# Kernel optimization log

Measured on AMD Instinct MI355X. Metric: run time of the kernel, lower is better.

The kernel has to match this reference:

```python
import jax, jax.numpy as jnp
import numpy as np

N_NODES = 50000
N_EDGES = 800000
EMBED_DIM = 128
VOCAB = 30000
BATCH = 1024
CTX_LEN = 50
NUM_LAYERS = 2
BN_EPS = 1e-5


def setup_inputs() -> dict:
    key = jax.random.key(0)
    ks = jax.random.split(key, 20)
    D = EMBED_DIM
    edge_index = jax.random.randint(ks[0], (2, N_EDGES), 0, N_NODES)
    norm = jax.random.uniform(ks[1], (N_EDGES,), dtype=jnp.float32) * 0.2  # GCN deg^-1/2 * deg^-1/2 weights
    ctx_ids = jax.random.randint(ks[2], (BATCH, CTX_LEN), 0, VOCAB)
    miss_ids = jax.random.randint(ks[3], (BATCH,), 0, VOCAB)
    vocab_to_fg = jnp.where(
        jax.random.uniform(ks[4], (VOCAB,)) < 0.5,
        jax.random.randint(ks[5], (VOCAB,), 0, N_NODES),
        -1,
    )
    emb_table = jax.random.normal(ks[6], (VOCAB, D), dtype=jnp.float32) * 0.02
    emb_table = emb_table.at[0].set(0.0)  # padding_idx=0
    fg_emb = jax.random.normal(ks[7], (N_NODES, D), dtype=jnp.float32) * 0.02
    gc_w = jax.random.normal(ks[8], (NUM_LAYERS, D, D), dtype=jnp.float32) * 0.02
    bn_gamma = jnp.ones((NUM_LAYERS, D), dtype=jnp.float32)
    bn_beta = jnp.zeros((NUM_LAYERS, D), dtype=jnp.float32)
    attn_w = jax.random.normal(ks[9], (D,), dtype=jnp.float32) * 0.02
    attn_b = jnp.zeros((), dtype=jnp.float32)
    fusion_w = jax.random.normal(ks[10], (D, 2 * D), dtype=jnp.float32) * 0.02
    fusion_b = jnp.zeros((D,), dtype=jnp.float32)
    proj1_w = jax.random.normal(ks[11], (2 * D, 2 * D), dtype=jnp.float32) * 0.02
    proj1_b = jnp.zeros((2 * D,), dtype=jnp.float32)
    proj2_w = jax.random.normal(ks[12], (D, 2 * D), dtype=jnp.float32) * 0.02
    proj2_b = jnp.zeros((D,), dtype=jnp.float32)
    return dict(edge_index=edge_index, norm=norm, ctx_ids=ctx_ids, miss_ids=miss_ids,
                vocab_to_fg=vocab_to_fg, emb_table=emb_table, fg_emb=fg_emb, gc_w=gc_w,
                bn_gamma=bn_gamma, bn_beta=bn_beta, attn_w=attn_w, attn_b=attn_b,
                fusion_w=fusion_w, fusion_b=fusion_b, proj1_w=proj1_w, proj1_b=proj1_b,
                proj2_w=proj2_w, proj2_b=proj2_b)


def reference(edge_index, norm, ctx_ids, miss_ids, vocab_to_fg, emb_table, fg_emb,
              gc_w, bn_gamma, bn_beta, attn_w, attn_b, fusion_w, fusion_b,
              proj1_w, proj1_b, proj2_w, proj2_b):
    N, D = fg_emb.shape
    row, col = edge_index[0], edge_index[1]
    # --- GCN stack: h <- h + BN(ReLU(Linear(A @ h))) ---
    h = fg_emb
    for l in range(gc_w.shape[0]):
        # sparse adj matmul: out[i] = sum_{(i,j) in E} norm_e * h[j]
        agg = jax.ops.segment_sum(norm[:, None] * h[col], row, num_segments=N)  # [N, D]
        z = jax.nn.relu(agg @ gc_w[l].T)
        mu = jnp.mean(z, axis=0)
        var = jnp.var(z, axis=0)  # biased, matches BN train-mode normalization
        h2 = (z - mu) * jax.lax.rsqrt(var + BN_EPS) * bn_gamma[l] + bn_beta[l]
        h = h + h2  # dropout is identity in eval reference
    graph_embs = h
    # --- context attention pooling ---
    ctx = emb_table[ctx_ids]                      # [B, L, D]
    logits = jnp.einsum('bld,d->bl', ctx, attn_w) + attn_b
    w = jax.nn.softmax(logits, axis=1)
    ctx_emb = jnp.einsum('bl,bld->bd', w, ctx)    # [B, D]
    # --- missing-ingredient embedding: vocab emb fused with gathered graph emb ---
    base = emb_table[miss_ids]                    # [B, D]
    fg_ids = vocab_to_fg[miss_ids]
    mask = fg_ids >= 0
    gp = jnp.where(mask[:, None], graph_embs[jnp.clip(fg_ids, 0)], 0.0)
    miss_emb = jnp.concatenate([base, gp], axis=-1) @ fusion_w.T + fusion_b
    # --- projection MLP ---
    q = jnp.concatenate([ctx_emb, miss_emb], axis=-1)
    q = jax.nn.relu(q @ proj1_w.T + proj1_b)
    query = q @ proj2_w.T + proj2_b
    return query, graph_embs
```

## Files before the change

### kernel.cpp

```cpp
#include <hip/hip_runtime.h>

#define NN 50000
#define NE 800000
#define DIM 128
#define NB 1024
#define CTXL 50
#define BN_EPS 1e-5f
#define STRIPS 3125
#define GEMM_BLOCKS 512
#define NBK 49
#define BCAP 20000
#define ABLK 1024
#define NAB 782

static const size_t OFF_Z    = 0;
static const size_t OFF_AH   = 6400000;
static const size_t OFF_HBF  = 9600000;
static const size_t OFF_EDG  = 12800000;
static const size_t OFF_RS   = 14400000;
static const size_t OFF_SCSH = 14550400;
static const size_t OFF_WH   = 14550656;
static const size_t OFF_WL   = 14567040;
static const size_t OFF_BKT  = OFF_Z + 3200000;
static const size_t OFF_P2   = OFF_Z + 3200000;
static const size_t OFF_ACNT = OFF_AH;
static const size_t OFF_AOFS = OFF_AH + 40000;
static const size_t OFF_BTOT = OFF_AH + 80000;
static const size_t OFF_QIN  = OFF_Z;
static const size_t OFF_CAT  = OFF_Z + 131072;
static const size_t OFF_Q1   = OFF_Z + 262144;
static const size_t OFF_FWB  = OFF_Z + 393216;
static const size_t OFF_P1B  = OFF_Z + 409600;
static const size_t OFF_P2B  = OFF_Z + 442368;

typedef __attribute__((ext_vector_type(8))) short s16x8;
typedef __attribute__((ext_vector_type(4))) float fx4;

__device__ __forceinline__ unsigned short f2bf(float f) {
    unsigned u = __float_as_uint(f);
    unsigned r = u + 0x7FFFu + ((u >> 16) & 1u);
    return (unsigned short)(r >> 16);
}
__device__ __forceinline__ float bf2f(unsigned short b) {
    return __uint_as_float((unsigned)b << 16);
}

__global__ __launch_bounds__(256) void csr_prep_kernel(const int* __restrict__ row,
                                                       const float* __restrict__ W,
                                                       const float* __restrict__ fg,
                                                       int* __restrict__ cnt,
                                                       unsigned short* __restrict__ Wh,
                                                       unsigned short* __restrict__ Wl,
                                                       unsigned short* __restrict__ hbf) {
    int i = blockIdx.x * 256 + threadIdx.x;
    if (i < 2 * DIM * DIM) {
        float v = W[i];
        unsigned short h = f2bf(v);
        Wh[i] = h;
        Wl[i] = f2bf(v - bf2f(h));
    }
    if (i < NN * DIM / 4) {
        float4 v = reinterpret_cast<const float4*>(fg)[i];
        reinterpret_cast<ushort4*>(hbf)[i] =
            make_ushort4(f2bf(v.x), f2bf(v.y), f2bf(v.z), f2bf(v.w));
    }
    if (blockIdx.x < NAB) {
        __shared__ int c[NBK];
        int t = threadIdx.x;
        if (t < NBK) c[t] = 0;
        __syncthreads();
        int base = blockIdx.x * ABLK;
        #pragma unroll
        for (int k = 0; k < 4; k++) {
            int e = base + k * 256 + t;
            if (e < NE) atomicAdd(&c[row[e] >> 10], 1);
        }
        __syncthreads();
        if (t < NBK) cnt[t * 784 + blockIdx.x] = c[t];
    }
}

__global__ __launch_bounds__(1024) void binA_scan(const int* __restrict__ cnt,
                                                  int* __restrict__ ofs,
                                                  int* __restrict__ btot) {
    __shared__ int lds[1024];
    int b = blockIdx.x, t = threadIdx.x;
    int v = (t < NAB) ? cnt[b * 784 + t] : 0;
    lds[t] = v;
    __syncthreads();
    for (int off = 1; off < 1024; off <<= 1) {
        int add = (t >= off) ? lds[t - off] : 0;
        __syncthreads();
        lds[t] += add;
        __syncthreads();
    }
    if (t < NAB) ofs[b * 784 + t] = lds[t] - v;
    if (t == NAB - 1) btot[b] = lds[t];
}

__global__ __launch_bounds__(256) void binA_scatter(const int* __restrict__ row,
                                                    const int* __restrict__ col,
                                                    const float* __restrict__ norm,
                                                    const int* __restrict__ ofs,
                                                    unsigned long long* __restrict__ bkt) {
    __shared__ int c[NBK], bofs[NBK], brsv[NBK];
    __shared__ unsigned long long stage[ABLK];
    __shared__ unsigned char stgb[ABLK];
    int t = threadIdx.x;
    if (t < NBK) c[t] = 0;
    __syncthreads();
    int base = blockIdx.x * ABLK;
    int my_b[4], my_i[4];
    unsigned long long my_pk[4];
    #pragma unroll
    for (int k = 0; k < 4; k++) {
        int e = base + k * 256 + t;
        if (e < NE) {
            int r = row[e];
            int b = r >> 10;
            my_b[k] = b;
            my_i[k] = atomicAdd(&c[b], 1);
            my_pk[k] = ((unsigned long long)__float_as_uint(norm[e]) << 32)
                     | ((unsigned long long)(unsigned)col[e] << 10)
                     | (unsigned)(r & 1023);
        } else my_b[k] = -1;
    }
    __syncthreads();
    if (t == 0) {
        int s = 0;
        for (int b = 0; b < NBK; b++) { bofs[b] = s; s += c[b]; }
    }
    if (t < NBK) brsv[t] = ofs[t * 784 + blockIdx.x];
    __syncthreads();
    #pragma unroll
    for (int k = 0; k < 4; k++) {
        if (my_b[k] >= 0) {
            int j = bofs[my_b[k]] + my_i[k];
            stage[j] = my_pk[k];
            stgb[j] = (unsigned char)my_b[k];
        }
    }
    __syncthreads();
    int tot = min(NE - base, ABLK);
    for (int j = t; j < tot; j += 256) {
        int b = stgb[j];
        int dst = brsv[b] + (j - bofs[b]);
        if (dst < BCAP) bkt[(size_t)b * BCAP + dst] = stage[j];
    }
}

__global__ __launch_bounds__(1024) void binB_kernel(const unsigned long long* __restrict__ bkt,
                                                    const int* __restrict__ btot,
                                                    int* __restrict__ row_start,
                                                    unsigned long long* __restrict__ edge_out) {
    __shared__ int c[1024];
    __shared__ int rs[1024];
    __shared__ int gofs_s;
    int b = blockIdx.x, t = threadIdx.x;
    c[t] = 0;
    if (t < 64) {
        int v = (t < b) ? btot[t] : 0;
        #pragma unroll
        for (int off = 32; off; off >>= 1) v += __shfl_down(v, off);
        if (t == 0) gofs_s = v;
    }
    __syncthreads();
    int n = btot[b];
    size_t bb = (size_t)b * BCAP;
    for (int i = t; i < n; i += 1024)
        atomicAdd(&c[(int)(bkt[bb + i] & 1023u)], 1);
    __syncthreads();
    int myc = c[t];
    for (int off = 1; off < 1024; off <<= 1) {
        int add = (t >= off) ? c[t - off] : 0;
        __syncthreads();
        c[t] += add;
        __syncthreads();
    }
    int excl = gofs_s + c[t] - myc;
    rs[t] = excl;
    int r = (b << 10) + t;
    if (r <= NN) row_start[r] = excl;
    __syncthreads();
    c[t] = 0;
    __syncthreads();
    for (int i = t; i < n; i += 1024) {
        unsigned long long pk = bkt[bb + i];
        int lr = (int)(pk & 1023u);
        unsigned colv = (unsigned)((pk >> 10) & 0xFFFFu);
        unsigned nrm = (unsigned)(pk >> 32);
        int k = atomicAdd(&c[lr], 1);
        edge_out[rs[lr] + k] = ((unsigned long long)nrm << 32) | colv;
    }
}

__global__ __launch_bounds__(256) void agg_bf_kernel(const unsigned short* __restrict__ hbf,
                                                     const int* __restrict__ row_start,
                                                     const float* __restrict__ edge_s,
                                                     unsigned short* __restrict__ Ah) {
    int gw = (blockIdx.x * 256 + threadIdx.x) >> 6;
    int lane = threadIdx.x & 63;
    int half = lane >> 5;
    int c4 = (lane & 31) * 4;
    if (gw >= NN) return;
    int s = row_start[gw];
    int e = row_start[gw + 1];
    const int2* ep = (const int2*)edge_s;
    float a0 = 0.f, a1 = 0.f, a2 = 0.f, a3 = 0.f;
    int j = s + half;
    for (; j + 6 < e; j += 8) {
        int2 p0 = ep[j], p1 = ep[j + 2], p2 = ep[j + 4], p3 = ep[j + 6];
        ushort4 v0 = *(const ushort4*)(hbf + (size_t)p0.x * DIM + c4);
        ushort4 v1 = *(const ushort4*)(hbf + (size_t)p1.x * DIM + c4);
        ushort4 v2 = *(const ushort4*)(hbf + (size_t)p2.x * DIM + c4);
        ushort4 v3 = *(const ushort4*)(hbf + (size_t)p3.x * DIM + c4);
        float w0 = __int_as_float(p0.y), w1 = __int_as_float(p1.y);
        float w2 = __int_as_float(p2.y), w3 = __int_as_float(p3.y);
        a0 = fmaf(w0, bf2f(v0.x), a0); a1 = fmaf(w0, bf2f(v0.y), a1);
        a2 = fmaf(w0, bf2f(v0.z), a2); a3 = fmaf(w0, bf2f(v0.w), a3);
        a0 = fmaf(w1, bf2f(v1.x), a0); a1 = fmaf(w1, bf2f(v1.y), a1);
        a2 = fmaf(w1, bf2f(v1.z), a2); a3 = fmaf(w1, bf2f(v1.w), a3);
        a0 = fmaf(w2, bf2f(v2.x), a0); a1 = fmaf(w2, bf2f(v2.y), a1);
        a2 = fmaf(w2, bf2f(v2.z), a2); a3 = fmaf(w2, bf2f(v2.w), a3);
        a0 = fmaf(w3, bf2f(v3.x), a0); a1 = fmaf(w3, bf2f(v3.y), a1);
        a2 = fmaf(w3, bf2f(v3.z), a2); a3 = fmaf(w3, bf2f(v3.w), a3);
    }
    for (; j < e; j += 2) {
        int2 p = ep[j];
        ushort4 v = *(const ushort4*)(hbf + (size_t)p.x * DIM + c4);
        float w = __int_as_float(p.y);
        a0 = fmaf(w, bf2f(v.x), a0); a1 = fmaf(w, bf2f(v.y), a1);
        a2 = fmaf(w, bf2f(v.z), a2); a3 = fmaf(w, bf2f(v.w), a3);
    }
    a0 += __shfl_xor(a0, 32); a1 += __shfl_xor(a1, 32);
    a2 += __shfl_xor(a2, 32); a3 += __shfl_xor(a3, 32);
    if (half == 0) {
        *(ushort4*)(Ah + (size_t)gw * DIM + c4) =
            make_ushort4(f2bf(a0), f2bf(a1), f2bf(a2), f2bf(a3));
    }
}

__global__ __launch_bounds__(256) void gemm_mfma_kernel(const unsigned short* __restrict__ Ah,
                                                        const unsigned short* __restrict__ Wh,
                                                        const unsigned short* __restrict__ Wl,
                                                        unsigned short* __restrict__ zb,
                                                        float* __restrict__ P2) {
    __shared__ __align__(16) short Wlds[2][128][128];
    int tid = threadIdx.x;
    int lane = tid & 63;
    int w = tid >> 6;
    int r16 = lane & 15;
    int kg = lane >> 4;

    #pragma unroll
    for (int ff = 0; ff < 16; ff++) {
        int f = ff * 256 + tid;
        int plane = f >> 11;
        int c = (f >> 4) & 127;
        int ck = f & 15;
        const unsigned short* srcp = (plane ? Wl : Wh) + (size_t)c * DIM + ck * 8;
        *(s16x8*)&Wlds[plane][c][(ck ^ (c & 7)) * 8] = *(const s16x8*)srcp;
    }
    __syncthreads();

    float bsum[2][4] = {{0.f}}, bsq[2][4] = {{0.f}};

    for (int strip = blockIdx.x; strip < STRIPS; strip += GEMM_BLOCKS) {
        size_t abase = (size_t)(strip * 16 + r16) * DIM + kg * 8;
        s16x8 b[4];
        #pragma unroll
        for (int ks = 0; ks < 4; ks++) b[ks] = *(const s16x8*)(Ah + abase + ks * 32);

        fx4 acc[2];
        acc[0] = (fx4){0.f, 0.f, 0.f, 0.f};
        acc[1] = (fx4){0.f, 0.f, 0.f, 0.f};
        #pragma unroll
        for (int ks = 0; ks < 4; ks++) {
            #pragma unroll
            for (int ct = 0; ct < 2; ct++) {
                int wrow = w * 32 + ct * 16 + r16;
                int wch = ((ks * 4 + kg) ^ (r16 & 7)) * 8;
                s16x8 wh8 = *(const s16x8*)&Wlds[0][wrow][wch];
                s16x8 wl8 = *(const s16x8*)&Wlds[1][wrow][wch];
                acc[ct] = __builtin_amdgcn_mfma_f32_16x16x32_bf16(wh8, b[ks], acc[ct], 0, 0, 0);
                acc[ct] = __builtin_amdgcn_mfma_f32_16x16x32_bf16(wl8, b[ks], acc[ct], 0, 0, 0);
            }
        }
        size_t zrow = (size_t)(strip * 16 + r16) * DIM + w * 32 + kg * 4;
        #pragma unroll
        for (int ct = 0; ct < 2; ct++) {
            float x0 = fmaxf(acc[ct][0], 0.f);
            float x1 = fmaxf(acc[ct][1], 0.f);
            float x2 = fmaxf(acc[ct][2], 0.f);
            float x3 = fmaxf(acc[ct][3], 0.f);
            bsum[ct][0] += x0; bsq[ct][0] += x0 * x0;
            bsum[ct][1] += x1; bsq[ct][1] += x1 * x1;
            bsum[ct][2] += x2; bsq[ct][2] += x2 * x2;
            bsum[ct][3] += x3; bsq[ct][3] += x3 * x3;
            *(ushort4*)(zb + zrow + ct * 16) = make_ushort4(f2bf(x0), f2bf(x1), f2bf(x2), f2bf(x3));
        }
    }

    #pragma unroll
    for (int ct = 0; ct < 2; ct++) {
        #pragma unroll
        for (int jj = 0; jj < 4; jj++) {
            float s = bsum[ct][jj], q = bsq[ct][jj];
            #pragma unroll
            for (int off = 1; off <= 8; off <<= 1) {
                s += __shfl_xor(s, off);
                q += __shfl_xor(q, off);
            }
            if (r16 == 0) {
                int ch = w * 32 + ct * 16 + kg * 4 + jj;
                P2[blockIdx.x * 256 + ch] = s;
                P2[blockIdx.x * 256 + 128 + ch] = q;
            }
        }
    }
}

__global__ __launch_bounds__(1024) void bn_finalize_kernel(const float* __restrict__ P2,
                                                           const float* __restrict__ gamma,
                                                           const float* __restrict__ beta,
                                                           float* __restrict__ scsh) {
    __shared__ float tot[4][256];
    int t = threadIdx.x & 255;
    int g = threadIdx.x >> 8;
    float a0 = 0.f, a1 = 0.f, a2 = 0.f, a3 = 0.f;
    int base = g * (GEMM_BLOCKS / 4);
    for (int bx = 0; bx < GEMM_BLOCKS / 4; bx += 4) {
        a0 += P2[(size_t)(base + bx + 0) * 256 + t];
        a1 += P2[(size_t)(base + bx + 1) * 256 + t];
        a2 += P2[(size_t)(base + bx + 2) * 256 + t];
        a3 += P2[(size_t)(base + bx + 3) * 256 + t];
    }
    tot[g][t] = (a0 + a1) + (a2 + a3);
    __syncthreads();
    if (threadIdx.x < 128) {
        int c = threadIdx.x;
        float sum = (tot[0][c] + tot[1][c]) + (tot[2][c] + tot[3][c]);
        float sq  = (tot[0][128 + c] + tot[1][128 + c]) + (tot[2][128 + c] + tot[3][128 + c]);
        float mu = sum * (1.f / (float)NN);
        float var = sq * (1.f / (float)NN) - mu * mu;
        float sc = gamma[c] / sqrtf(var + BN_EPS);
        scsh[c] = sc;
        scsh[128 + c] = beta[c] - mu * sc;
    }
}

__global__ __launch_bounds__(256) void residual_kernel(const float* hin,
                                                       const unsigned short* zb,
                                                       const float* __restrict__ scsh,
                                                       float* hout,
                                                       unsigned short* hbf_out) {
    int i = blockIdx.x * 256 + threadIdx.x;
    if (i >= NN * DIM / 4) return;
    int c = (i * 4) & 127;
    ushort4 z4 = reinterpret_cast<const ushort4*>(zb)[i];
    float4 hv = reinterpret_cast<const float4*>(hin)[i];
    float4 sc = *reinterpret_cast<const float4*>(scsh + c);
    float4 sh = *reinterpret_cast<const float4*>(scsh + 128 + c);
    float4 o;
    o.x = hv.x + bf2f(z4.x) * sc.x + sh.x;
    o.y = hv.y + bf2f(z4.y) * sc.y + sh.y;
    o.z = hv.z + bf2f(z4.z) * sc.z + sh.z;
    o.w = hv.w + bf2f(z4.w) * sc.w + sh.w;
    reinterpret_cast<float4*>(hout)[i] = o;
    if (hbf_out) {
        ushort4 ob = make_ushort4(f2bf(o.x), f2bf(o.y), f2bf(o.z), f2bf(o.w));
        reinterpret_cast<ushort4*>(hbf_out)[i] = ob;
    }
}

__global__ __launch_bounds__(256) void pool_kernel(const int* __restrict__ ctx_ids,
                                                   const int* __restrict__ miss_ids,
                                                   const int* __restrict__ vocab_to_fg,
                                                   const float* __restrict__ emb_table,
                                                   const float* __restrict__ graph,
                                                   const float* __restrict__ attn_w,
                                                   const float* __restrict__ attn_b,
                                                   const float* __restrict__ fusion_w,
                                                   const float* __restrict__ proj1_w,
                                                   const float* __restrict__ proj2_w,
                                                   unsigned short* __restrict__ qinb,
                                                   unsigned short* __restrict__ catb,
                                                   unsigned short* __restrict__ fwb,
                                                   unsigned short* __restrict__ p1b,
                                                   unsigned short* __restrict__ p2b) {
    int b = blockIdx.x;
    int tid = threadIdx.x;
    __shared__ float ctx[CTXL][129];
    __shared__ float aw[128];
    __shared__ float lg[64];

    if (tid < 128) {
        int i = b * 128 + tid;
        if (i < 32768) fwb[i] = f2bf(fusion_w[i]);
        else if (i < 98304) p1b[i - 32768] = f2bf(proj1_w[i - 32768]);
        else p2b[i - 98304] = f2bf(proj2_w[i - 98304]);
    }

    if (tid < 128) aw[tid] = attn_w[tid];
    for (int f = tid; f < CTXL * 32; f += 256) {
        int t = f >> 5, d4 = (f & 31) * 4;
        int vid = ctx_ids[b * CTXL + t];
        float4 v = *(const float4*)(emb_table + (size_t)vid * DIM + d4);
        ctx[t][d4 + 0] = v.x; ctx[t][d4 + 1] = v.y;
        ctx[t][d4 + 2] = v.z; ctx[t][d4 + 3] = v.w;
    }
    __syncthreads();

    if (tid < CTXL) {
        float s = 0.f;
        for (int k = 0; k < 128; k++) s += ctx[tid][k] * aw[k];
        lg[tid] = s + attn_b[0];
    }
    __syncthreads();

    if (tid < 64) {
        float v = (tid < CTXL) ? lg[tid] : -INFINITY;
        float m = v;
        for (int off = 32; off; off >>= 1) m = fmaxf(m, __shfl_xor(m, off));
        float e = (tid < CTXL) ? expf(v - m) : 0.f;
        float s = e;
        for (int off = 32; off; off >>= 1) s += __shfl_xor(s, off);
        if (tid < CTXL) lg[tid] = e / s;
    }
    __syncthreads();

    int mid = miss_ids[b];
    if (tid < 128) {
        float s = 0.f;
        for (int t = 0; t < CTXL; t++) s += lg[t] * ctx[t][tid];
        qinb[(size_t)b * 256 + tid] = f2bf(s);
        catb[(size_t)b * 256 + tid] = f2bf(emb_table[(size_t)mid * DIM + tid]);
    } else {
        int d = tid - 128;
        int fg = vocab_to_fg[mid];
        float gp = (fg >= 0) ? graph[(size_t)fg * DIM + d] : 0.f;
        catb[(size_t)b * 256 + tid] = f2bf(gp);
    }
}

__global__ __launch_bounds__(256) void head_gemm_kernel(const unsigned short* __restrict__ A,
                                                        const unsigned short* __restrict__ W,
                                                        const float* __restrict__ bias,
                                                        unsigned short* __restrict__ outb,
                                                        float* __restrict__ outf,
                                                        int ocol, int ostride, int relu) {
    __shared__ __align__(16) short Wlds[64][256];
    int tid = threadIdx.x;
    int lane = tid & 63;
    int r16 = lane & 15;
    int kg = lane >> 4;
    int cgb = blockIdx.y * 64;

    #pragma unroll
    for (int ff = 0; ff < 8; ff++) {
        int f = ff * 256 + tid;
        int c = f >> 5;
        int ck = f & 31;
        s16x8 v = *(const s16x8*)(W + (size_t)(cgb + c) * 256 + ck * 8);
        *(s16x8*)&Wlds[c][(ck ^ (c & 7)) * 8] = v;
    }
    __syncthreads();

    int w = tid >> 6;
    int row = blockIdx.x * 16 + r16;

    size_t abase = (size_t)row * 256 + kg * 8;
    s16x8 bfrag[8];
    #pragma unroll
    for (int ks = 0; ks < 8; ks++) bfrag[ks] = *(const s16x8*)(A + abase + ks * 32);

    fx4 acc = (fx4){0.f, 0.f, 0.f, 0.f};
    int wrow = w * 16 + r16;
    #pragma unroll
    for (int ks = 0; ks < 8; ks++) {
        int wch = (((ks * 4 + kg) ^ (r16 & 7))) * 8;
        s16x8 w8 = *(const s16x8*)&Wlds[wrow][wch];
        acc = __builtin_amdgcn_mfma_f32_16x16x32_bf16(w8, bfrag[ks], acc, 0, 0, 0);
    }

    int cbase = cgb + w * 16 + kg * 4;
    float4 o;
    o.x = acc[0] + bias[cbase + 0];
    o.y = acc[1] + bias[cbase + 1];
    o.z = acc[2] + bias[cbase + 2];
    o.w = acc[3] + bias[cbase + 3];
    if (relu) {
        o.x = fmaxf(o.x, 0.f); o.y = fmaxf(o.y, 0.f);
        o.z = fmaxf(o.z, 0.f); o.w = fmaxf(o.w, 0.f);
    }
    size_t op = (size_t)row * ostride + ocol + cbase;
    if (outb) {
        *(ushort4*)(outb + op) = make_ushort4(f2bf(o.x), f2bf(o.y), f2bf(o.z), f2bf(o.w));
    } else {
        *(float4*)(outf + op) = o;
    }
}

extern "C" void kernel_launch(void* const* d_in, const int* in_sizes, int n_in,
                              void* d_out, int out_size, void* d_ws, size_t ws_size,
                              hipStream_t stream) {
    const int*   edge_index = (const int*)d_in[0];
    const float* norm       = (const float*)d_in[1];
    const int*   ctx_ids    = (const int*)d_in[2];
    const int*   miss_ids   = (const int*)d_in[3];
    const int*   vocab_to_fg= (const int*)d_in[4];
    const float* emb_table  = (const float*)d_in[5];
    const float* fg_emb     = (const float*)d_in[6];
    const float* gc_w       = (const float*)d_in[7];
    const float* bn_gamma   = (const float*)d_in[8];
    const float* bn_beta    = (const float*)d_in[9];
    const float* attn_w     = (const float*)d_in[10];
    const float* attn_b     = (const float*)d_in[11];
    const float* fusion_w   = (const float*)d_in[12];
    const float* fusion_b   = (const float*)d_in[13];
    const float* proj1_w    = (const float*)d_in[14];
    const float* proj1_b    = (const float*)d_in[15];
    const float* proj2_w    = (const float*)d_in[16];
    const float* proj2_b    = (const float*)d_in[17];

    const int* row = edge_index;
    const int* col = edge_index + NE;

    float* ws = (float*)d_ws;
    unsigned short* zb     = (unsigned short*)(ws + OFF_Z);
    unsigned short* Ah     = (unsigned short*)(ws + OFF_AH);
    unsigned short* hbf    = (unsigned short*)(ws + OFF_HBF);
    float*          edge_s = ws + OFF_EDG;
    int*   row_start = (int*)(ws + OFF_RS);
    float* scsh      = ws + OFF_SCSH;
    unsigned short* Wh = (unsigned short*)(ws + OFF_WH);
    unsigned short* Wl = (unsigned short*)(ws + OFF_WL);
    float* P2        = ws + OFF_P2;
    unsigned long long* bkt = (unsigned long long*)(ws + OFF_BKT);
    int*   acnt      = (int*)(ws + OFF_ACNT);
    int*   aofs      = (int*)(ws + OFF_AOFS);
    int*   btot      = (int*)(ws + OFF_BTOT);
    unsigned short* qinb = (unsigned short*)(ws + OFF_QIN);
    unsigned short* catb = (unsigned short*)(ws + OFF_CAT);
    unsigned short* q1b  = (unsigned short*)(ws + OFF_Q1);
    unsigned short* fwb  = (unsigned short*)(ws + OFF_FWB);
    unsigned short* p1b  = (unsigned short*)(ws + OFF_P1B);
    unsigned short* p2b  = (unsigned short*)(ws + OFF_P2B);

    float* query = (float*)d_out;
    float* G     = (float*)d_out + (size_t)NB * DIM;

    csr_prep_kernel<<<6250, 256, 0, stream>>>(row, gc_w, fg_emb, acnt, Wh, Wl, hbf);
    binA_scan<<<NBK, 1024, 0, stream>>>(acnt, aofs, btot);
    binA_scatter<<<NAB, 256, 0, stream>>>(row, col, norm, aofs, bkt);
    binB_kernel<<<NBK, 1024, 0, stream>>>(bkt, btot, row_start, (unsigned long long*)edge_s);

    const int AGG_B = NN / 4;
    const int RES_B = (NN * DIM / 4) / 256;

    agg_bf_kernel<<<AGG_B, 256, 0, stream>>>(hbf, row_start, edge_s, Ah);
    gemm_mfma_kernel<<<GEMM_BLOCKS, 256, 0, stream>>>(Ah, Wh, Wl, zb, P2);
    bn_finalize_kernel<<<1, 1024, 0, stream>>>(P2, bn_gamma, bn_beta, scsh);
    residual_kernel<<<RES_B, 256, 0, stream>>>(fg_emb, zb, scsh, G, hbf);

    agg_bf_kernel<<<AGG_B, 256, 0, stream>>>(hbf, row_start, edge_s, Ah);
    gemm_mfma_kernel<<<GEMM_BLOCKS, 256, 0, stream>>>(Ah, Wh + DIM * DIM, Wl + DIM * DIM, zb, P2);
    bn_finalize_kernel<<<1, 1024, 0, stream>>>(P2, bn_gamma + 128, bn_beta + 128, scsh);
    residual_kernel<<<RES_B, 256, 0, stream>>>(G, zb, scsh, G, nullptr);

    pool_kernel<<<NB, 256, 0, stream>>>(ctx_ids, miss_ids, vocab_to_fg, emb_table, G,
                                        attn_w, attn_b, fusion_w, proj1_w, proj2_w,
                                        qinb, catb, fwb, p1b, p2b);
    dim3 hg2(64, 2), hg4(64, 4);
    head_gemm_kernel<<<hg2, 256, 0, stream>>>(catb, fwb, fusion_b, qinb, nullptr, 128, 256, 0);
    head_gemm_kernel<<<hg4, 256, 0, stream>>>(qinb, p1b, proj1_b, q1b, nullptr, 0, 256, 1);
    head_gemm_kernel<<<hg2, 256, 0, stream>>>(q1b, p2b, proj2_b, nullptr, query, 0, 128, 0);
}
```

Before: 192.6 us.

## Fuse head GEMMs, atomically reduce BN stats, keep residual state in bf16

Merges the three small head GEMM launches into one kernel that keeps intermediate activations and each weight matrix in LDS. BN partial sums are now atomically accumulated into 32 rows, which are zeroed in the prep kernel and again after each finalize, so the finalize kernel reads far less. The residual path now reads and writes only the bf16 node state, and writes the fp32 graph output only after the last layer. This cuts fp32 traffic but rounds fg_emb and the layer-1 output to bf16. The aggregation loop is also unrolled to 8 outstanding gathers per half-wave.

```diff
diff --git a/kernel.cpp b/kernel.cpp
--- a/kernel.cpp
+++ b/kernel.cpp
@@ -18,17 +18,16 @@
 static const size_t OFF_HBF  = 9600000;
 static const size_t OFF_EDG  = 12800000;
 static const size_t OFF_RS   = 14400000;
+static const size_t OFF_P2   = 14450048;
 static const size_t OFF_SCSH = 14550400;
 static const size_t OFF_WH   = 14550656;
 static const size_t OFF_WL   = 14567040;
 static const size_t OFF_BKT  = OFF_Z + 3200000;
-static const size_t OFF_P2   = OFF_Z + 3200000;
 static const size_t OFF_ACNT = OFF_AH;
 static const size_t OFF_AOFS = OFF_AH + 40000;
 static const size_t OFF_BTOT = OFF_AH + 80000;
 static const size_t OFF_QIN  = OFF_Z;
 static const size_t OFF_CAT  = OFF_Z + 131072;
-static const size_t OFF_Q1   = OFF_Z + 262144;
 static const size_t OFF_FWB  = OFF_Z + 393216;
 static const size_t OFF_P1B  = OFF_Z + 409600;
 static const size_t OFF_P2B  = OFF_Z + 442368;
@@ -51,7 +50,8 @@
                                                        int* __restrict__ cnt,
                                                        unsigned short* __restrict__ Wh,
                                                        unsigned short* __restrict__ Wl,
-                                                       unsigned short* __restrict__ hbf) {
+                                                       unsigned short* __restrict__ hbf,
+                                                       float* __restrict__ P2) {
     int i = blockIdx.x * 256 + threadIdx.x;
     if (i < 2 * DIM * DIM) {
         float v = W[i];
@@ -63,6 +63,9 @@
         float4 v = reinterpret_cast<const float4*>(fg)[i];
         reinterpret_cast<ushort4*>(hbf)[i] =
             make_ushort4(f2bf(v.x), f2bf(v.y), f2bf(v.z), f2bf(v.w));
+    }
+    if (blockIdx.x >= 6218) {
+        P2[(blockIdx.x - 6218) * 256 + threadIdx.x] = 0.f;
     }
     if (blockIdx.x < NAB) {
         __shared__ int c[NBK];
@@ -208,22 +211,19 @@
     const int2* ep = (const int2*)edge_s;
     float a0 = 0.f, a1 = 0.f, a2 = 0.f, a3 = 0.f;
     int j = s + half;
-    for (; j + 6 < e; j += 8) {
-        int2 p0 = ep[j], p1 = ep[j + 2], p2 = ep[j + 4], p3 = ep[j + 6];
-        ushort4 v0 = *(const ushort4*)(hbf + (size_t)p0.x * DIM + c4);
-        ushort4 v1 = *(const ushort4*)(hbf + (size_t)p1.x * DIM + c4);
-        ushort4 v2 = *(const ushort4*)(hbf + (size_t)p2.x * DIM + c4);
-        ushort4 v3 = *(const ushort4*)(hbf + (size_t)p3.x * DIM + c4);
-        float w0 = __int_as_float(p0.y), w1 = __int_as_float(p1.y);
-        float w2 = __int_as_float(p2.y), w3 = __int_as_float(p3.y);
-        a0 = fmaf(w0, bf2f(v0.x), a0); a1 = fmaf(w0, bf2f(v0.y), a1);
-        a2 = fmaf(w0, bf2f(v0.z), a2); a3 = fmaf(w0, bf2f(v0.w), a3);
-        a0 = fmaf(w1, bf2f(v1.x), a0); a1 = fmaf(w1, bf2f(v1.y), a1);
-        a2 = fmaf(w1, bf2f(v1.z), a2); a3 = fmaf(w1, bf2f(v1.w), a3);
-        a0 = fmaf(w2, bf2f(v2.x), a0); a1 = fmaf(w2, bf2f(v2.y), a1);
-        a2 = fmaf(w2, bf2f(v2.z), a2); a3 = fmaf(w2, bf2f(v2.w), a3);
-        a0 = fmaf(w3, bf2f(v3.x), a0); a1 = fmaf(w3, bf2f(v3.y), a1);
-        a2 = fmaf(w3, bf2f(v3.z), a2); a3 = fmaf(w3, bf2f(v3.w), a3);
+    for (; j + 14 < e; j += 16) {
+        int2 p[8];
+        ushort4 v[8];
+        #pragma unroll
+        for (int k = 0; k < 8; k++) p[k] = ep[j + 2 * k];
+        #pragma unroll
+        for (int k = 0; k < 8; k++) v[k] = *(const ushort4*)(hbf + (size_t)p[k].x * DIM + c4);
+        #pragma unroll
+        for (int k = 0; k < 8; k++) {
+            float w = __int_as_float(p[k].y);
+            a0 = fmaf(w, bf2f(v[k].x), a0); a1 = fmaf(w, bf2f(v[k].y), a1);
+            a2 = fmaf(w, bf2f(v[k].z), a2); a3 = fmaf(w, bf2f(v[k].w), a3);
+        }
     }
     for (; j < e; j += 2) {
         int2 p = ep[j];
@@ -301,6 +301,7 @@
         }
     }
 
+    int prow = (blockIdx.x & 31) * 256;
     #pragma unroll
     for (int ct = 0; ct < 2; ct++) {
         #pragma unroll
@@ -313,63 +314,58 @@
             }
             if (r16 == 0) {
                 int ch = w * 32 + ct * 16 + kg * 4 + jj;
-                P2[blockIdx.x * 256 + ch] = s;
-                P2[blockIdx.x * 256 + 128 + ch] = q;
+                unsafeAtomicAdd(&P2[prow + ch], s);
+                unsafeAtomicAdd(&P2[prow + 128 + ch], q);
             }
         }
     }
 }
 
-__global__ __launch_bounds__(1024) void bn_finalize_kernel(const float* __restrict__ P2,
-                                                           const float* __restrict__ gamma,
-                                                           const float* __restrict__ beta,
-                                                           float* __restrict__ scsh) {
-    __shared__ float tot[4][256];
-    int t = threadIdx.x & 255;
-    int g = threadIdx.x >> 8;
-    float a0 = 0.f, a1 = 0.f, a2 = 0.f, a3 = 0.f;
-    int base = g * (GEMM_BLOCKS / 4);
-    for (int bx = 0; bx < GEMM_BLOCKS / 4; bx += 4) {
-        a0 += P2[(size_t)(base + bx + 0) * 256 + t];
-        a1 += P2[(size_t)(base + bx + 1) * 256 + t];
-        a2 += P2[(size_t)(base + bx + 2) * 256 + t];
-        a3 += P2[(size_t)(base + bx + 3) * 256 + t];
-    }
-    tot[g][t] = (a0 + a1) + (a2 + a3);
-    __syncthreads();
-    if (threadIdx.x < 128) {
-        int c = threadIdx.x;
-        float sum = (tot[0][c] + tot[1][c]) + (tot[2][c] + tot[3][c]);
-        float sq  = (tot[0][128 + c] + tot[1][128 + c]) + (tot[2][128 + c] + tot[3][128 + c]);
+__global__ __launch_bounds__(256) void bn_finalize_kernel(float* __restrict__ P2,
+                                                          const float* __restrict__ gamma,
+                                                          const float* __restrict__ beta,
+                                                          float* __restrict__ scsh) {
+    __shared__ float tot[256];
+    int t = threadIdx.x;
+    float s = 0.f;
+    #pragma unroll
+    for (int r = 0; r < 32; r++) s += P2[r * 256 + t];
+    tot[t] = s;
+    __syncthreads();
+    if (t < 128) {
+        float sum = tot[t];
+        float sq  = tot[128 + t];
         float mu = sum * (1.f / (float)NN);
         float var = sq * (1.f / (float)NN) - mu * mu;
-        float sc = gamma[c] / sqrtf(var + BN_EPS);
-        scsh[c] = sc;
-        scsh[128 + c] = beta[c] - mu * sc;
-    }
-}
-
-__global__ __launch_bounds__(256) void residual_kernel(const float* hin,
-                                                       const unsigned short* zb,
+        float sc = gamma[t] / sqrtf(var + BN_EPS);
+        scsh[t] = sc;
+        scsh[128 + t] = beta[t] - mu * sc;
+    }
+    #pragma unroll
+    for (int r = 0; r < 32; r++) P2[r * 256 + t] = 0.f;
+}
+
+__global__ __launch_bounds__(256) void residual_kernel(unsigned short* __restrict__ hbf,
+                                                       const unsigned short* __restrict__ zb,
                                                        const float* __restrict__ scsh,
-                                                       float* hout,
-                                                       unsigned short* hbf_out) {
+                                                       float* __restrict__ Gout) {
     int i = blockIdx.x * 256 + threadIdx.x;
     if (i >= NN * DIM / 4) return;
     int c = (i * 4) & 127;
     ushort4 z4 = reinterpret_cast<const ushort4*>(zb)[i];
-    float4 hv = reinterpret_cast<const float4*>(hin)[i];
+    ushort4 h4 = reinterpret_cast<const ushort4*>(hbf)[i];
     float4 sc = *reinterpret_cast<const float4*>(scsh + c);
     float4 sh = *reinterpret_cast<const float4*>(scsh + 128 + c);
     float4 o;
-    o.x = hv.x + bf2f(z4.x) * sc.x + sh.x;
-    o.y = hv.y + bf2f(z4.y) * sc.y + sh.y;
-    o.z = hv.z + bf2f(z4.z) * sc.z + sh.z;
-    o.w = hv.w + bf2f(z4.w) * sc.w + sh.w;
-    reinterpret_cast<float4*>(hout)[i] = o;
-    if (hbf_out) {
-        ushort4 ob = make_ushort4(f2bf(o.x), f2bf(o.y), f2bf(o.z), f2bf(o.w));
-        reinterpret_cast<ushort4*>(hbf_out)[i] = ob;
+    o.x = bf2f(h4.x) + bf2f(z4.x) * sc.x + sh.x;
+    o.y = bf2f(h4.y) + bf2f(z4.y) * sc.y + sh.y;
+    o.z = bf2f(h4.z) + bf2f(z4.z) * sc.z + sh.z;
+    o.w = bf2f(h4.w) + bf2f(z4.w) * sc.w + sh.w;
+    if (Gout) {
+        reinterpret_cast<float4*>(Gout)[i] = o;
+    } else {
+        reinterpret_cast<ushort4*>(hbf)[i] =
+            make_ushort4(f2bf(o.x), f2bf(o.y), f2bf(o.z), f2bf(o.w));
     }
 }
 
@@ -443,61 +439,133 @@
     }
 }
 
-__global__ __launch_bounds__(256) void head_gemm_kernel(const unsigned short* __restrict__ A,
-                                                        const unsigned short* __restrict__ W,
-                                                        const float* __restrict__ bias,
-                                                        unsigned short* __restrict__ outb,
-                                                        float* __restrict__ outf,
-                                                        int ocol, int ostride, int relu) {
-    __shared__ __align__(16) short Wlds[64][256];
+__global__ __launch_bounds__(256) void head_fused_kernel(const unsigned short* __restrict__ qinb,
+                                                         const unsigned short* __restrict__ catb,
+                                                         const unsigned short* __restrict__ fwb,
+                                                         const unsigned short* __restrict__ p1b,
+                                                         const unsigned short* __restrict__ p2b,
+                                                         const float* __restrict__ fusion_b,
+                                                         const float* __restrict__ proj1_b,
+                                                         const float* __restrict__ proj2_b,
+                                                         float* __restrict__ query) {
+    __shared__ __align__(16) short WL[65536];
+    __shared__ __align__(16) short qs[16][256];
+    __shared__ __align__(16) short q1s[16][256];
     int tid = threadIdx.x;
     int lane = tid & 63;
+    int w = tid >> 6;
     int r16 = lane & 15;
     int kg = lane >> 4;
-    int cgb = blockIdx.y * 64;
-
-    #pragma unroll
-    for (int ff = 0; ff < 8; ff++) {
+    int row = blockIdx.x * 16 + r16;
+
+    {
+        int r = tid >> 4, ck = tid & 15;
+        s16x8 v = *(const s16x8*)(qinb + (size_t)(blockIdx.x * 16 + r) * 256 + ck * 8);
+        *(s16x8*)&qs[r][(ck ^ (r & 7)) * 8] = v;
+    }
+    #pragma unroll
+    for (int ff = 0; ff < 16; ff++) {
         int f = ff * 256 + tid;
-        int c = f >> 5;
-        int ck = f & 31;
-        s16x8 v = *(const s16x8*)(W + (size_t)(cgb + c) * 256 + ck * 8);
-        *(s16x8*)&Wlds[c][(ck ^ (c & 7)) * 8] = v;
-    }
-    __syncthreads();
-
-    int w = tid >> 6;
-    int row = blockIdx.x * 16 + r16;
-
-    size_t abase = (size_t)row * 256 + kg * 8;
-    s16x8 bfrag[8];
-    #pragma unroll
-    for (int ks = 0; ks < 8; ks++) bfrag[ks] = *(const s16x8*)(A + abase + ks * 32);
-
-    fx4 acc = (fx4){0.f, 0.f, 0.f, 0.f};
-    int wrow = w * 16 + r16;
+        int c = f >> 5, ck = f & 31;
+        s16x8 v = *(const s16x8*)(fwb + (size_t)c * 256 + ck * 8);
+        *(s16x8*)&WL[c * 256 + (ck ^ (c & 7)) * 8] = v;
+    }
+    s16x8 af[8];
+    {
+        size_t abase = (size_t)row * 256 + kg * 8;
+        #pragma unroll
+        for (int ks = 0; ks < 8; ks++) af[ks] = *(const s16x8*)(catb + abase + ks * 32);
+    }
+    __syncthreads();
+
+    #pragma unroll
+    for (int ct = 0; ct < 2; ct++) {
+        fx4 acc = (fx4){0.f, 0.f, 0.f, 0.f};
+        int wrow = w * 32 + ct * 16 + r16;
+        #pragma unroll
+        for (int ks = 0; ks < 8; ks++) {
+            int wch = ((ks * 4 + kg) ^ (r16 & 7)) * 8;
+            s16x8 w8 = *(const s16x8*)&WL[wrow * 256 + wch];
+            acc = __builtin_amdgcn_mfma_f32_16x16x32_bf16(w8, af[ks], acc, 0, 0, 0);
+        }
+        int cbase = w * 32 + ct * 16 + kg * 4;
+        float x0 = acc[0] + fusion_b[cbase + 0];
+        float x1 = acc[1] + fusion_b[cbase + 1];
+        float x2 = acc[2] + fusion_b[cbase + 2];
+        float x3 = acc[3] + fusion_b[cbase + 3];
+        int col = 128 + cbase;
+        int c8 = col >> 3, off = col & 7;
+        *(ushort4*)&qs[r16][(c8 ^ (r16 & 7)) * 8 + off] =
+            make_ushort4(f2bf(x0), f2bf(x1), f2bf(x2), f2bf(x3));
+    }
+    __syncthreads();
+
+    #pragma unroll
+    for (int ff = 0; ff < 32; ff++) {
+        int f = ff * 256 + tid;
+        int c = f >> 5, ck = f & 31;
+        s16x8 v = *(const s16x8*)(p1b + (size_t)c * 256 + ck * 8);
+        *(s16x8*)&WL[c * 256 + (ck ^ (c & 7)) * 8] = v;
+    }
     #pragma unroll
     for (int ks = 0; ks < 8; ks++) {
-        int wch = (((ks * 4 + kg) ^ (r16 & 7))) * 8;
-        s16x8 w8 = *(const s16x8*)&Wlds[wrow][wch];
-        acc = __builtin_amdgcn_mfma_f32_16x16x32_bf16(w8, bfrag[ks], acc, 0, 0, 0);
-    }
-
-    int cbase = cgb + w * 16 + kg * 4;
-    float4 o;
-    o.x = acc[0] + bias[cbase + 0];
-    o.y = acc[1] + bias[cbase + 1];
-    o.z = acc[2] + bias[cbase + 2];
-    o.w = acc[3] + bias[cbase + 3];
-    if (relu) {
-        o.x = fmaxf(o.x, 0.f); o.y = fmaxf(o.y, 0.f);
-        o.z = fmaxf(o.z, 0.f); o.w = fmaxf(o.w, 0.f);
-    }
-    size_t op = (size_t)row * ostride + ocol + cbase;
-    if (outb) {
-        *(ushort4*)(outb + op) = make_ushort4(f2bf(o.x), f2bf(o.y), f2bf(o.z), f2bf(o.w));
-    } else {
-        *(float4*)(outf + op) = o;
+        int c8 = kg + ks * 4;
+        af[ks] = *(const s16x8*)&qs[r16][(c8 ^ (r16 & 7)) * 8];
+    }
+    __syncthreads();
+
+    #pragma unroll
+    for (int ct = 0; ct < 4; ct++) {
+        fx4 acc = (fx4){0.f, 0.f, 0.f, 0.f};
+        int wrow = w * 64 + ct * 16 + r16;
+        #pragma unroll
+        for (int ks = 0; ks < 8; ks++) {
+            int wch = ((ks * 4 + kg) ^ (r16 & 7)) * 8;
+            s16x8 w8 = *(const s16x8*)&WL[wrow * 256 + wch];
+            acc = __builtin_amdgcn_mfma_f32_16x16x32_bf16(w8, af[ks], acc, 0, 0, 0);
+        }
+        int cbase = w * 64 + ct * 16 + kg * 4;
+        float x0 = fmaxf(acc[0] + proj1_b[cbase + 0], 0.f);
+        float x1 = fmaxf(acc[1] + proj1_b[cbase + 1], 0.f);
+        float x2 = fmaxf(acc[2] + proj1_b[cbase + 2], 0.f);
+        float x3 = fmaxf(acc[3] + proj1_b[cbase + 3], 0.f);
+        int c8 = cbase >> 3, off = cbase & 7;
+        *(ushort4*)&q1s[r16][(c8 ^ (r16 & 7)) * 8 + off] =
+            make_ushort4(f2bf(x0), f2bf(x1), f2bf(x2), f2bf(x3));
+    }
+    __syncthreads();
+
+    #pragma unroll
+    for (int ff = 0; ff < 16; ff++) {
+        int f = ff * 256 + tid;
+        int c = f >> 5, ck = f & 31;
+        s16x8 v = *(const s16x8*)(p2b + (size_t)c * 256 + ck * 8);
+        *(s16x8*)&WL[c * 256 + (ck ^ (c & 7)) * 8] = v;
+    }
+    #pragma unroll
+    for (int ks = 0; ks < 8; ks++) {
+        int c8 = kg + ks * 4;
+        af[ks] = *(const s16x8*)&q1s[r16][(c8 ^ (r16 & 7)) * 8];
+    }
+    __syncthreads();
+
+    #pragma unroll
+    for (int ct = 0; ct < 2; ct++) {
+        fx4 acc = (fx4){0.f, 0.f, 0.f, 0.f};
+        int wrow = w * 32 + ct * 16 + r16;
+        #pragma unroll
+        for (int ks = 0; ks < 8; ks++) {
+            int wch = ((ks * 4 + kg) ^ (r16 & 7)) * 8;
+            s16x8 w8 = *(const s16x8*)&WL[wrow * 256 + wch];
+            acc = __builtin_amdgcn_mfma_f32_16x16x32_bf16(w8, af[ks], acc, 0, 0, 0);
+        }
+        int cbase = w * 32 + ct * 16 + kg * 4;
+        float4 o;
+        o.x = acc[0] + proj2_b[cbase + 0];
+        o.y = acc[1] + proj2_b[cbase + 1];
+        o.z = acc[2] + proj2_b[cbase + 2];
+        o.w = acc[3] + proj2_b[cbase + 3];
+        *(float4*)(query + (size_t)row * 128 + cbase) = o;
     }
 }
 
@@ -532,17 +600,16 @@
     unsigned short* hbf    = (unsigned short*)(ws + OFF_HBF);
     float*          edge_s = ws + OFF_EDG;
     int*   row_start = (int*)(ws + OFF_RS);
+    float* P2        = ws + OFF_P2;
     float* scsh      = ws + OFF_SCSH;
     unsigned short* Wh = (unsigned short*)(ws + OFF_WH);
     unsigned short* Wl = (unsigned short*)(ws + OFF_WL);
-    float* P2        = ws + OFF_P2;
     unsigned long long* bkt = (unsigned long long*)(ws + OFF_BKT);
     int*   acnt      = (int*)(ws + OFF_ACNT);
     int*   aofs      = (int*)(ws + OFF_AOFS);
     int*   btot      = (int*)(ws + OFF_BTOT);
     unsigned short* qinb = (unsigned short*)(ws + OFF_QIN);
     unsigned short* catb = (unsigned short*)(ws + OFF_CAT);
-    unsigned short* q1b  = (unsigned short*)(ws + OFF_Q1);
     unsigned short* fwb  = (unsigned short*)(ws + OFF_FWB);
     unsigned short* p1b  = (unsigned short*)(ws + OFF_P1B);
     unsigned short* p2b  = (unsigned short*)(ws + OFF_P2B);
@@ -550,7 +617,7 @@
     float* query = (float*)d_out;
     float* G     = (float*)d_out + (size_t)NB * DIM;
 
-    csr_prep_kernel<<<6250, 256, 0, stream>>>(row, gc_w, fg_emb, acnt, Wh, Wl, hbf);
+    csr_prep_kernel<<<6250, 256, 0, stream>>>(row, gc_w, fg_emb, acnt, Wh, Wl, hbf, P2);
     binA_scan<<<NBK, 1024, 0, stream>>>(acnt, aofs, btot);
     binA_scatter<<<NAB, 256, 0, stream>>>(row, col, norm, aofs, bkt);
     binB_kernel<<<NBK, 1024, 0, stream>>>(bkt, btot, row_start, (unsigned long long*)edge_s);
@@ -560,19 +627,17 @@
 
     agg_bf_kernel<<<AGG_B, 256, 0, stream>>>(hbf, row_start, edge_s, Ah);
     gemm_mfma_kernel<<<GEMM_BLOCKS, 256, 0, stream>>>(Ah, Wh, Wl, zb, P2);
-    bn_finalize_kernel<<<1, 1024, 0, stream>>>(P2, bn_gamma, bn_beta, scsh);
-    residual_kernel<<<RES_B, 256, 0, stream>>>(fg_emb, zb, scsh, G, hbf);
+    bn_finalize_kernel<<<1, 256, 0, stream>>>(P2, bn_gamma, bn_beta, scsh);
+    residual_kernel<<<RES_B, 256, 0, stream>>>(hbf, zb, scsh, nullptr);
 
     agg_bf_kernel<<<AGG_B, 256, 0, stream>>>(hbf, row_start, edge_s, Ah);
     gemm_mfma_kernel<<<GEMM_BLOCKS, 256, 0, stream>>>(Ah, Wh + DIM * DIM, Wl + DIM * DIM, zb, P2);
-    bn_finalize_kernel<<<1, 1024, 0, stream>>>(P2, bn_gamma + 128, bn_beta + 128, scsh);
-    residual_kernel<<<RES_B, 256, 0, stream>>>(G, zb, scsh, G, nullptr);
+    bn_finalize_kernel<<<1, 256, 0, stream>>>(P2, bn_gamma + 128, bn_beta + 128, scsh);
+    residual_kernel<<<RES_B, 256, 0, stream>>>(hbf, zb, scsh, G);
 
     pool_kernel<<<NB, 256, 0, stream>>>(ctx_ids, miss_ids, vocab_to_fg, emb_table, G,
                                         attn_w, attn_b, fusion_w, proj1_w, proj2_w,
                                         qinb, catb, fwb, p1b, p2b);
-    dim3 hg2(64, 2), hg4(64, 4);
-    head_gemm_kernel<<<hg2, 256, 0, stream>>>(catb, fwb, fusion_b, qinb, nullptr, 128, 256, 0);
-    head_gemm_kernel<<<hg4, 256, 0, stream>>>(qinb, p1b, proj1_b, q1b, nullptr, 0, 256, 1);
-    head_gemm_kernel<<<hg2, 256, 0, stream>>>(q1b, p2b, proj2_b, nullptr, query, 0, 128, 0);
-}
+    head_fused_kernel<<<64, 256, 0, stream>>>(qinb, catb, fwb, p1b, p2b,
+                                              fusion_b, proj1_b, proj2_b, query);
+}
```

Result: no change. 194.2 us (+0.8%).
